# Optimization experiments

Hardware: AMD Instinct MI355X
Metric: run time of the kernel (lower is better)

The kernel has to match this reference:

```python
import jax, jax.numpy as jnp
import numpy as np

TEMP = 0.1
EPS = 0.5
N, D, P = 8192, 128, 1


def setup_inputs() -> dict:
    key = jax.random.key(0)
    k1, k2 = jax.random.split(key)
    return {
        "embeddings": jax.random.normal(k1, (N, D), dtype=jnp.float32),
        "properties": jax.random.uniform(k2, (N, P), dtype=jnp.float32),
    }


def reference(embeddings, properties):
    n = embeddings.shape[0]
    # L2-normalize rows, cosine similarity scaled by temperature
    e = embeddings / jnp.linalg.norm(embeddings, axis=1, keepdims=True)
    sim = (e @ e.T) / TEMP  # [N, N]

    # mask from property distances; comparison is non-differentiable in torch,
    # so stop_gradient keeps the jax graph identical (and avoids sqrt(0) nans)
    props = jax.lax.stop_gradient(properties)
    pd2 = jnp.sum((props[:, None, :] - props[None, :, :]) ** 2, axis=-1)  # [N, N]
    # torch.cdist(p=2) gives sqrt(pd2); code then takes .sqrt() again -> pd2**0.25
    prop_dists = jnp.sqrt(jnp.sqrt(pd2)) + 1e-8
    mask = (prop_dists < EPS).astype(sim.dtype)

    eye = jnp.eye(n, dtype=bool)
    mask = jnp.where(eye, 0.0, mask)          # fill_diagonal_(0)
    logits = jnp.where(eye, -1e9, sim)        # fill_diagonal_(-1e9)
    log_probs = jax.nn.log_softmax(logits, axis=1)

    # fused masked per-row mean of -log_probs over positives, then mean over
    # rows that have at least one positive (replaces the python loop)
    counts = mask.sum(axis=1)                      # [N]
    valid = counts > 0
    per_row = -(mask * log_probs).sum(axis=1) / jnp.maximum(counts, 1.0)
    n_valid = valid.sum()
    loss = jnp.where(
        n_valid > 0,
        jnp.sum(jnp.where(valid, per_row, 0.0)) / jnp.maximum(n_valid, 1).astype(per_row.dtype),
        jnp.asarray(0.0, dtype=per_row.dtype),
    )
    return loss
```

## Files before the change

kernel.cpp:

```cpp
#include <hip/hip_runtime.h>
#include <hip/hip_bf16.h>

#define N_ROWS 8192
#define DIM 128

typedef short v8s  __attribute__((ext_vector_type(8)));
typedef float v16f __attribute__((ext_vector_type(16)));
typedef float v2f  __attribute__((ext_vector_type(2)));
typedef unsigned int u32;

constexpr int NS = 16;
constexpr int CW = N_ROWS / NS;
constexpr int NSLOT = NS;
constexpr int TILE_J = 32;
constexpr int NT = CW / TILE_J;
constexpr int TB = TILE_J * DIM * 2;
constexpr int BI = 256;
constexpr float T2 = 0.0625f;
constexpr float C1 = 14.426950408889634f;

#define GLDS(gptr, lptr, sz)                                                   \
  __builtin_amdgcn_global_load_lds(                                            \
      (const __attribute__((address_space(1))) u32*)(gptr),                    \
      (__attribute__((address_space(3))) u32*)(lptr), sz, 0, 0)

__device__ __forceinline__ unsigned short f2bf(float f) {
  __hip_bfloat16 h = __float2bfloat16(f);
  return __builtin_bit_cast(unsigned short, h);
}

__global__ __launch_bounds__(256) void knorm(const float* __restrict__ emb,
                                             unsigned short* __restrict__ ebf) {
  const int row  = blockIdx.x * 4 + (threadIdx.x >> 6);
  const int lane = threadIdx.x & 63;
  const float2 v = *reinterpret_cast<const float2*>(emb + (size_t)row * DIM + lane * 2);
  float ss = fmaf(v.x, v.x, v.y * v.y);
#pragma unroll
  for (int off = 32; off > 0; off >>= 1) ss += __shfl_xor(ss, off);
  const float rn = 1.0f / sqrtf(ss);
  const unsigned int packed =
      (unsigned int)f2bf(v.x * rn) | ((unsigned int)f2bf(v.y * rn) << 16);
  *reinterpret_cast<unsigned int*>(ebf + (size_t)row * DIM + lane * 2) = packed;
}

__global__ __launch_bounds__(512) void kmain(const unsigned short* __restrict__ ebf,
                                             const float* __restrict__ props,
                                             float* __restrict__ part) {
  const int tid  = threadIdx.x;
  const int lane = tid & 63;
  const int w    = tid >> 6;
  const int r31  = lane & 31;
  const int hi   = lane >> 5;
  const int i0   = blockIdx.x * BI;
  const int iw0  = i0 + w * 32;
  const int jbase = blockIdx.y * CW;

  __shared__ __align__(1024) char sA[2 * TB + CW * 4];
  char* sprops = sA + 2 * TB;

  const int icol = iw0 + r31;

  v8s bfr[8];
#pragma unroll
  for (int kk = 0; kk < 8; ++kk)
    bfr[kk] = *reinterpret_cast<const v8s*>(ebf + (size_t)icol * DIM + kk * 16 + hi * 8);
  const float pc = props[icol];

  GLDS(props + jbase + tid, sprops + w * 256, 4);

  auto stageA = [&](char* base, int tile) {
    const int jrow0 = jbase + tile * TILE_J;
    const int row   = w * 4 + (lane >> 4);
    const int colb  = ((lane & 15) << 4) ^ ((row & 7) << 4);
    GLDS(ebf + (size_t)(jrow0 + row) * DIM + (colb >> 1), base + w * 1024, 16);
  };

  const int phase = (blockIdx.x * 5) & (NT - 1);
  stageA(sA, phase);
  __syncthreads();

  v2f es2 = {0.f, 0.f}, ms2 = {0.f, 0.f}, ct2 = {0.f, 0.f};
  const int rswz = (r31 & 7) << 4;
  const v2f c1v = {C1, C1}, mc1v = {-C1, -C1}, pc2 = {pc, pc};

  for (int t = 0; t < NT; ++t) {
    const int tt = (t + phase) & (NT - 1);
    if (t + 1 < NT) stageA(sA + ((t + 1) & 1) * TB, (tt + 1) & (NT - 1));

    char* base = sA + (t & 1) * TB;
    const int jrow0 = jbase + tt * TILE_J;

    v8s af[8];
#pragma unroll
    for (int kk = 0; kk < 8; ++kk)
      af[kk] = *reinterpret_cast<const v8s*>(
          base + r31 * 256 + ((kk * 32 + hi * 16) ^ rswz));

    v16f acc = {0.f, 0.f, 0.f, 0.f, 0.f, 0.f, 0.f, 0.f,
                0.f, 0.f, 0.f, 0.f, 0.f, 0.f, 0.f, 0.f};
#pragma unroll
    for (int kk = 0; kk < 8; ++kk)
      acc = __builtin_amdgcn_mfma_f32_32x32x16_bf16(af[kk], bfr[kk], acc, 0, 0, 0);

    if ((unsigned)(jrow0 - i0) < (unsigned)BI) {
#pragma unroll
      for (int r = 0; r < 8; ++r) {
        const int row0 = ((2 * r) & 3) + 8 * (r >> 1) + 4 * hi;
        const v2f pj2  = *reinterpret_cast<const v2f*>(
            sprops + ((size_t)tt * 32 + row0) * 4);
        const v2f dot2 = {acc[2 * r], acc[2 * r + 1]};
        const v2f arg  = __builtin_elementwise_fma(dot2, c1v, mc1v);
        const float ex0 = __builtin_amdgcn_exp2f(arg.x);
        const float ex1 = __builtin_amdgcn_exp2f(arg.y);
        const int jr0 = jrow0 + row0;
        const bool neq0 = (jr0 != icol), neq1 = (jr0 + 1 != icol);
        const v2f exv = {neq0 ? ex0 : 0.f, neq1 ? ex1 : 0.f};
        es2 += exv;
        const v2f d = pc2 - pj2, dsq = d * d;
        const v2f msk = {(neq0 && dsq.x < T2) ? 1.f : 0.f,
                         (neq1 && dsq.y < T2) ? 1.f : 0.f};
        ct2 += msk;
        ms2 = __builtin_elementwise_fma(msk, dot2, ms2);
      }
    } else {
#pragma unroll
      for (int r = 0; r < 8; ++r) {
        const int row0 = ((2 * r) & 3) + 8 * (r >> 1) + 4 * hi;
        const v2f pj2  = *reinterpret_cast<const v2f*>(
            sprops + ((size_t)tt * 32 + row0) * 4);
        const v2f dot2 = {acc[2 * r], acc[2 * r + 1]};
        const v2f arg  = __builtin_elementwise_fma(dot2, c1v, mc1v);
        const v2f exv  = {__builtin_amdgcn_exp2f(arg.x), __builtin_amdgcn_exp2f(arg.y)};
        es2 += exv;
        const v2f d = pc2 - pj2, dsq = d * d;
        const v2f msk = {(dsq.x < T2) ? 1.f : 0.f, (dsq.y < T2) ? 1.f : 0.f};
        ct2 += msk;
        ms2 = __builtin_elementwise_fma(msk, dot2, ms2);
      }
    }
    __syncthreads();
  }

  float es = es2.x + es2.y, ms = ms2.x + ms2.y, ct = ct2.x + ct2.y;
  es += __shfl_xor(es, 32);
  ms += __shfl_xor(ms, 32);
  ct += __shfl_xor(ct, 32);

  if (hi == 0) {
    float* p0 = part + (size_t)blockIdx.y * 3 * N_ROWS;
    p0[icol]              = es;
    p0[N_ROWS + icol]     = ms;
    p0[2 * N_ROWS + icol] = ct;
  }
}

__global__ __launch_bounds__(64) void kreduce(const float* __restrict__ part,
                                              float* __restrict__ bs,
                                              float* __restrict__ bc) {
  const int row = blockIdx.x * 64 + threadIdx.x;
  float es = 0.f, ms = 0.f, ct = 0.f;
#pragma unroll
  for (int sp = 0; sp < NSLOT; ++sp) {
    const float* p0 = part + (size_t)sp * 3 * N_ROWS;
    es += p0[row];
    ms += p0[N_ROWS + row];
    ct += p0[2 * N_ROWS + row];
  }
  const float lse = 10.0f + logf(es);
  const float per = (ct * lse - 10.0f * ms) / fmaxf(ct, 1.0f);
  float val = (ct > 0.f) ? per : 0.f;
  float vld = (ct > 0.f) ? 1.f : 0.f;
#pragma unroll
  for (int off = 32; off > 0; off >>= 1) {
    val += __shfl_xor(val, off);
    vld += __shfl_xor(vld, off);
  }
  if (threadIdx.x == 0) {
    bs[blockIdx.x] = val;
    bc[blockIdx.x] = vld;
  }
}

__global__ __launch_bounds__(64) void kfin(const float* __restrict__ bs,
                                           const float* __restrict__ bc,
                                           float* __restrict__ out) {
  const int l = threadIdx.x;
  float s = bs[l] + bs[l + 64];
  float c = bc[l] + bc[l + 64];
#pragma unroll
  for (int off = 32; off > 0; off >>= 1) {
    s += __shfl_xor(s, off);
    c += __shfl_xor(c, off);
  }
  if (l == 0) out[0] = (c > 0.f) ? (s / c) : 0.f;
}

extern "C" void kernel_launch(void* const* d_in, const int* in_sizes, int n_in,
                              void* d_out, int out_size, void* d_ws, size_t ws_size,
                              hipStream_t stream) {
  const float* emb   = (const float*)d_in[0];
  const float* props = (const float*)d_in[1];
  float* out = (float*)d_out;

  unsigned short* ebf = (unsigned short*)d_ws;
  const size_t EBF_BYTES  = (size_t)N_ROWS * DIM * 2;
  const size_t PART_BYTES = (size_t)NSLOT * 3 * N_ROWS * 4;
  float* part = (float*)((char*)d_ws + EBF_BYTES);
  float* bs   = (float*)((char*)d_ws + EBF_BYTES + PART_BYTES);
  float* bc   = bs + 128;

  knorm<<<N_ROWS / 4, 256, 0, stream>>>(emb, ebf);
  kmain<<<dim3(N_ROWS / BI, NS), 512, 0, stream>>>(ebf, props, part);
  kreduce<<<N_ROWS / 64, 64, 0, stream>>>(part, bs, bc);
  kfin<<<1, 64, 0, stream>>>(bs, bc, out);
}
```

Before: 45.60 us.

## Give each wave two 32-column i-tiles to reuse staged j-tiles

Each wave now holds B fragments for 64 i-columns instead of 32 and issues two MFMA chains per staged 32-row j-tile, doubling the block's i-extent to 512. Every LDS-staged j-tile and A-fragment read is reused across twice as many outputs, which halves the global-to-LDS traffic per unit of work and the grid's x dimension. In exchange register pressure roughly doubles for fragments and accumulators, and the grid shrinks to 256 blocks, which may lower occupancy or leave CUs underused.

Result: slower. 51.80 us (+13.6%).

```diff
diff --git a/kernel.cpp b/kernel.cpp
--- a/kernel.cpp
+++ b/kernel.cpp
@@ -15,7 +15,7 @@
 constexpr int TILE_J = 32;
 constexpr int NT = CW / TILE_J;
 constexpr int TB = TILE_J * DIM * 2;
-constexpr int BI = 256;
+constexpr int BI = 512;
 constexpr float T2 = 0.0625f;
 constexpr float C1 = 14.426950408889634f;
 
@@ -52,19 +52,23 @@
   const int r31  = lane & 31;
   const int hi   = lane >> 5;
   const int i0   = blockIdx.x * BI;
-  const int iw0  = i0 + w * 32;
+  const int iw0  = i0 + w * 64;
   const int jbase = blockIdx.y * CW;
 
   __shared__ __align__(1024) char sA[2 * TB + CW * 4];
   char* sprops = sA + 2 * TB;
 
-  const int icol = iw0 + r31;
-
-  v8s bfr[8];
-#pragma unroll
-  for (int kk = 0; kk < 8; ++kk)
-    bfr[kk] = *reinterpret_cast<const v8s*>(ebf + (size_t)icol * DIM + kk * 16 + hi * 8);
-  const float pc = props[icol];
+  const int icol0 = iw0 + r31;
+  const int icol1 = iw0 + 32 + r31;
+
+  v8s bfr0[8], bfr1[8];
+#pragma unroll
+  for (int kk = 0; kk < 8; ++kk) {
+    bfr0[kk] = *reinterpret_cast<const v8s*>(ebf + (size_t)icol0 * DIM + kk * 16 + hi * 8);
+    bfr1[kk] = *reinterpret_cast<const v8s*>(ebf + (size_t)icol1 * DIM + kk * 16 + hi * 8);
+  }
+  const float pc0 = props[icol0];
+  const float pc1 = props[icol1];
 
   GLDS(props + jbase + tid, sprops + w * 256, 4);
 
@@ -79,9 +83,11 @@
   stageA(sA, phase);
   __syncthreads();
 
-  v2f es2 = {0.f, 0.f}, ms2 = {0.f, 0.f}, ct2 = {0.f, 0.f};
+  v2f es0 = {0.f, 0.f}, ms0 = {0.f, 0.f}, ct0 = {0.f, 0.f};
+  v2f es1 = {0.f, 0.f}, ms1 = {0.f, 0.f}, ct1 = {0.f, 0.f};
   const int rswz = (r31 & 7) << 4;
-  const v2f c1v = {C1, C1}, mc1v = {-C1, -C1}, pc2 = {pc, pc};
+  const v2f c1v = {C1, C1}, mc1v = {-C1, -C1};
+  const v2f pc02 = {pc0, pc0}, pc12 = {pc1, pc1};
 
   for (int t = 0; t < NT; ++t) {
     const int tt = (t + phase) & (NT - 1);
@@ -96,11 +102,14 @@
       af[kk] = *reinterpret_cast<const v8s*>(
           base + r31 * 256 + ((kk * 32 + hi * 16) ^ rswz));
 
-    v16f acc = {0.f, 0.f, 0.f, 0.f, 0.f, 0.f, 0.f, 0.f,
-                0.f, 0.f, 0.f, 0.f, 0.f, 0.f, 0.f, 0.f};
-#pragma unroll
-    for (int kk = 0; kk < 8; ++kk)
-      acc = __builtin_amdgcn_mfma_f32_32x32x16_bf16(af[kk], bfr[kk], acc, 0, 0, 0);
+    v16f acc0 = {0.f, 0.f, 0.f, 0.f, 0.f, 0.f, 0.f, 0.f,
+                 0.f, 0.f, 0.f, 0.f, 0.f, 0.f, 0.f, 0.f};
+    v16f acc1 = acc0;
+#pragma unroll
+    for (int kk = 0; kk < 8; ++kk) {
+      acc0 = __builtin_amdgcn_mfma_f32_32x32x16_bf16(af[kk], bfr0[kk], acc0, 0, 0, 0);
+      acc1 = __builtin_amdgcn_mfma_f32_32x32x16_bf16(af[kk], bfr1[kk], acc1, 0, 0, 0);
+    }
 
     if ((unsigned)(jrow0 - i0) < (unsigned)BI) {
 #pragma unroll
@@ -108,19 +117,33 @@
         const int row0 = ((2 * r) & 3) + 8 * (r >> 1) + 4 * hi;
         const v2f pj2  = *reinterpret_cast<const v2f*>(
             sprops + ((size_t)tt * 32 + row0) * 4);
-        const v2f dot2 = {acc[2 * r], acc[2 * r + 1]};
-        const v2f arg  = __builtin_elementwise_fma(dot2, c1v, mc1v);
-        const float ex0 = __builtin_amdgcn_exp2f(arg.x);
-        const float ex1 = __builtin_amdgcn_exp2f(arg.y);
         const int jr0 = jrow0 + row0;
-        const bool neq0 = (jr0 != icol), neq1 = (jr0 + 1 != icol);
-        const v2f exv = {neq0 ? ex0 : 0.f, neq1 ? ex1 : 0.f};
-        es2 += exv;
-        const v2f d = pc2 - pj2, dsq = d * d;
-        const v2f msk = {(neq0 && dsq.x < T2) ? 1.f : 0.f,
-                         (neq1 && dsq.y < T2) ? 1.f : 0.f};
-        ct2 += msk;
-        ms2 = __builtin_elementwise_fma(msk, dot2, ms2);
+        {
+          const v2f dot2 = {acc0[2 * r], acc0[2 * r + 1]};
+          const v2f arg  = __builtin_elementwise_fma(dot2, c1v, mc1v);
+          const bool neq0 = (jr0 != icol0), neq1 = (jr0 + 1 != icol0);
+          const v2f exv = {neq0 ? __builtin_amdgcn_exp2f(arg.x) : 0.f,
+                           neq1 ? __builtin_amdgcn_exp2f(arg.y) : 0.f};
+          es0 += exv;
+          const v2f d = pc02 - pj2, dsq = d * d;
+          const v2f msk = {(neq0 && dsq.x < T2) ? 1.f : 0.f,
+                           (neq1 && dsq.y < T2) ? 1.f : 0.f};
+          ct0 += msk;
+          ms0 = __builtin_elementwise_fma(msk, dot2, ms0);
+        }
+        {
+          const v2f dot2 = {acc1[2 * r], acc1[2 * r + 1]};
+          const v2f arg  = __builtin_elementwise_fma(dot2, c1v, mc1v);
+          const bool neq0 = (jr0 != icol1), neq1 = (jr0 + 1 != icol1);
+          const v2f exv = {neq0 ? __builtin_amdgcn_exp2f(arg.x) : 0.f,
+                           neq1 ? __builtin_amdgcn_exp2f(arg.y) : 0.f};
+          es1 += exv;
+          const v2f d = pc12 - pj2, dsq = d * d;
+          const v2f msk = {(neq0 && dsq.x < T2) ? 1.f : 0.f,
+                           (neq1 && dsq.y < T2) ? 1.f : 0.f};
+          ct1 += msk;
+          ms1 = __builtin_elementwise_fma(msk, dot2, ms1);
+        }
       }
     } else {
 #pragma unroll
@@ -128,29 +151,44 @@
         const int row0 = ((2 * r) & 3) + 8 * (r >> 1) + 4 * hi;
         const v2f pj2  = *reinterpret_cast<const v2f*>(
             sprops + ((size_t)tt * 32 + row0) * 4);
-        const v2f dot2 = {acc[2 * r], acc[2 * r + 1]};
-        const v2f arg  = __builtin_elementwise_fma(dot2, c1v, mc1v);
-        const v2f exv  = {__builtin_amdgcn_exp2f(arg.x), __builtin_amdgcn_exp2f(arg.y)};
-        es2 += exv;
-        const v2f d = pc2 - pj2, dsq = d * d;
-        const v2f msk = {(dsq.x < T2) ? 1.f : 0.f, (dsq.y < T2) ? 1.f : 0.f};
-        ct2 += msk;
-        ms2 = __builtin_elementwise_fma(msk, dot2, ms2);
+        {
+          const v2f dot2 = {acc0[2 * r], acc0[2 * r + 1]};
+          const v2f arg  = __builtin_elementwise_fma(dot2, c1v, mc1v);
+          const v2f exv  = {__builtin_amdgcn_exp2f(arg.x), __builtin_amdgcn_exp2f(arg.y)};
+          es0 += exv;
+          const v2f d = pc02 - pj2, dsq = d * d;
+          const v2f msk = {(dsq.x < T2) ? 1.f : 0.f, (dsq.y < T2) ? 1.f : 0.f};
+          ct0 += msk;
+          ms0 = __builtin_elementwise_fma(msk, dot2, ms0);
+        }
+        {
+          const v2f dot2 = {acc1[2 * r], acc1[2 * r + 1]};
+          const v2f arg  = __builtin_elementwise_fma(dot2, c1v, mc1v);
+          const v2f exv  = {__builtin_amdgcn_exp2f(arg.x), __builtin_amdgcn_exp2f(arg.y)};
+          es1 += exv;
+          const v2f d = pc12 - pj2, dsq = d * d;
+          const v2f msk = {(dsq.x < T2) ? 1.f : 0.f, (dsq.y < T2) ? 1.f : 0.f};
+          ct1 += msk;
+          ms1 = __builtin_elementwise_fma(msk, dot2, ms1);
+        }
       }
     }
     __syncthreads();
   }
 
-  float es = es2.x + es2.y, ms = ms2.x + ms2.y, ct = ct2.x + ct2.y;
-  es += __shfl_xor(es, 32);
-  ms += __shfl_xor(ms, 32);
-  ct += __shfl_xor(ct, 32);
+  float esa = es0.x + es0.y, msa = ms0.x + ms0.y, cta = ct0.x + ct0.y;
+  float esb = es1.x + es1.y, msb = ms1.x + ms1.y, ctb = ct1.x + ct1.y;
+  esa += __shfl_xor(esa, 32);  msa += __shfl_xor(msa, 32);  cta += __shfl_xor(cta, 32);
+  esb += __shfl_xor(esb, 32);  msb += __shfl_xor(msb, 32);  ctb += __shfl_xor(ctb, 32);
 
   if (hi == 0) {
     float* p0 = part + (size_t)blockIdx.y * 3 * N_ROWS;
-    p0[icol]              = es;
-    p0[N_ROWS + icol]     = ms;
-    p0[2 * N_ROWS + icol] = ct;
+    p0[icol0]              = esa;
+    p0[N_ROWS + icol0]     = msa;
+    p0[2 * N_ROWS + icol0] = cta;
+    p0[icol1]              = esb;
+    p0[N_ROWS + icol1]     = msb;
+    p0[2 * N_ROWS + icol1] = ctb;
   }
 }
 
```
